# Kernel tuning notes

Measured on AMD Instinct MI355X. Metric: run time of the kernel, lower is better.

## Reference

```python
import jax, jax.numpy as jnp
import numpy as np

D_MODEL = 1024
D_HIDDEN = 4096
D_OUT = 1024
N_EXPERTS = 8
TOP_K = 2
LOAD_BALANCE_WEIGHT = 0.01


def setup_inputs() -> dict:
    key = jax.random.key(0)
    ks = jax.random.split(key, 8)
    s = 0.02
    return {
        "input_tensor": jax.random.normal(ks[0], (4, 2048, D_MODEL), dtype=jnp.float32),
        "router_w": jax.random.normal(ks[1], (N_EXPERTS, D_MODEL), dtype=jnp.float32) * s,
        "router_b": jnp.zeros((N_EXPERTS,), dtype=jnp.float32),
        "w1": jax.random.normal(ks[2], (N_EXPERTS, D_HIDDEN, D_MODEL), dtype=jnp.float32) * s,
        "b1": jnp.zeros((N_EXPERTS, D_HIDDEN), dtype=jnp.float32),
        "w2": jax.random.normal(ks[3], (N_EXPERTS, D_OUT, D_HIDDEN), dtype=jnp.float32) * s,
        "b2": jnp.zeros((N_EXPERTS, D_OUT), dtype=jnp.float32),
    }


def _moe(input_tensor, router_w, router_b, w1, b1, w2, b2):
    B, S, D = input_tensor.shape
    x = input_tensor.reshape(-1, D)  # [T, D]
    T = x.shape[0]

    router_logits = x @ router_w.T + router_b          # [T, E]
    router_probs = jax.nn.softmax(router_logits, -1)   # [T, E]
    topk_w, topk_idx = jax.lax.top_k(router_probs, TOP_K)  # [T, K]
    topk_w = topk_w / jnp.sum(topk_w, axis=-1, keepdims=True)

    # Dense combine weights: zero for unselected experts (same math as
    # gather/scatter loop since unselected contributions get weight 0).
    combine = jnp.zeros((T, N_EXPERTS), dtype=topk_w.dtype)
    combine = combine.at[jnp.arange(T)[:, None], topk_idx].add(topk_w)  # [T, E]

    out = jnp.zeros((T, D_OUT), dtype=x.dtype)
    for e in range(N_EXPERTS):  # fixed, small expert loop
        h = jax.nn.relu(x @ w1[e].T + b1[e])      # [T, H]
        y = h @ w2[e].T + b2[e]                   # [T, O]
        out = out + combine[:, e:e + 1] * y
    output = out.reshape(B, S, D_OUT)

    # Load-balance loss
    one_hot = jax.nn.one_hot(topk_idx, N_EXPERTS, dtype=router_probs.dtype)  # [T, K, E]
    usage_frac = jnp.sum(one_hot, axis=(0, 1)) / (T * TOP_K)                 # [E]
    mean_prob = jnp.mean(router_probs, axis=0)                               # [E]
    lb_loss = LOAD_BALANCE_WEIGHT * N_EXPERTS * jnp.sum(usage_frac * mean_prob)
    return output, lb_loss


def reference(input_tensor, router_w, router_b, w1, b1, w2, b2):
    return _moe(input_tensor, router_w, router_b, w1, b1, w2, b2)
```

## Files before the change

kernel.cpp:

```cpp
#include <hip/hip_runtime.h>

typedef unsigned short u16;
typedef __bf16 bf16x8 __attribute__((ext_vector_type(8)));
typedef float f32x4 __attribute__((ext_vector_type(4)));

#define T_TOKENS 8192
#define DM 1024
#define DH 4096
#define DO 1024
#define NE 8

#define XB_OFF   0ull
#define W1B_OFF  16777216ull
#define W2B_OFF  16777216ull
#define H_OFF    83886080ull
#define PT_OFF   218103808ull
#define PG_OFF   218169344ull
#define TI_OFF   218234880ull
#define TG_OFF   218300416ull
#define ST_OFF   218365952ull


typedef __attribute__((address_space(3))) void lds_void;
typedef __attribute__((address_space(1))) const void gbl_void;

__device__ __forceinline__ void gload_lds16(const void* g, void* l) {
  __builtin_amdgcn_global_load_lds((gbl_void*)g, (lds_void*)l, 16, 0, 0);
}

__device__ __forceinline__ u16 f2bf(float f) {
  union { float f; unsigned u; } a; a.f = f;
  unsigned u = a.u;
  return (u16)((u + 0x7FFFu + ((u >> 16) & 1u)) >> 16);
}

__global__ __launch_bounds__(256) void cast_f32_bf16(const float* __restrict__ src,
                                                     u16* __restrict__ dst, int n4) {
  int i = blockIdx.x * 256 + threadIdx.x;
  if (i >= n4) return;
  float4 v = ((const float4*)src)[i];
  ushort4 o;
  o.x = f2bf(v.x); o.y = f2bf(v.y); o.z = f2bf(v.z); o.w = f2bf(v.w);
  ((ushort4*)dst)[i] = o;
}

__global__ __launch_bounds__(256) void router_kernel(
    const float* __restrict__ x, const float* __restrict__ rw,
    const float* __restrict__ rb,
    int* __restrict__ tidx, float* __restrict__ tgate,
    int* __restrict__ counts, float* __restrict__ psum)
{
  __shared__ float srw[NE * DM];
  __shared__ float s_psum[NE];
  __shared__ int s_cnt[NE];

  for (int i = threadIdx.x; i < NE * DM; i += 256) srw[i] = rw[i];
  if (threadIdx.x < NE) { s_psum[threadIdx.x] = 0.f; s_cnt[threadIdx.x] = 0; }
  __syncthreads();

  const int wave = threadIdx.x >> 6;
  const int lane = threadIdx.x & 63;
  const int t = blockIdx.x * 4 + wave;

  float xv[16];
#pragma unroll
  for (int i = 0; i < 16; i++) xv[i] = x[(size_t)t * DM + i * 64 + lane];

  float logits[8];
#pragma unroll
  for (int e = 0; e < 8; e++) {
    float p = 0.f;
#pragma unroll
    for (int i = 0; i < 16; i++) p += xv[i] * srw[e * DM + i * 64 + lane];
#pragma unroll
    for (int o = 32; o > 0; o >>= 1) p += __shfl_xor(p, o, 64);
    logits[e] = p;
  }

  if (lane == 0) {
    float pe[8];
    float mx = -1e30f;
    for (int e = 0; e < 8; e++) { logits[e] += rb[e]; mx = fmaxf(mx, logits[e]); }
    float s = 0.f;
    for (int e = 0; e < 8; e++) { pe[e] = expf(logits[e] - mx); s += pe[e]; }
    float inv = 1.f / s;
    for (int e = 0; e < 8; e++) { pe[e] *= inv; atomicAdd(&s_psum[e], pe[e]); }
    int i0 = 0;
    for (int e = 1; e < 8; e++) if (pe[e] > pe[i0]) i0 = e;
    int i1 = (i0 == 0) ? 1 : 0;
    for (int e = 0; e < 8; e++) if (e != i0 && pe[e] > pe[i1]) i1 = e;
    float g = pe[i0] + pe[i1];
    tidx[t * 2] = i0; tidx[t * 2 + 1] = i1;
    tgate[t * 2] = pe[i0] / g; tgate[t * 2 + 1] = pe[i1] / g;
    atomicAdd(&s_cnt[i0], 1); atomicAdd(&s_cnt[i1], 1);
  }
  __syncthreads();
  if (threadIdx.x < NE) {
    atomicAdd(&counts[threadIdx.x], s_cnt[threadIdx.x]);
    atomicAdd(&psum[threadIdx.x], s_psum[threadIdx.x]);
  }
}

__global__ void offsets_kernel(const int* __restrict__ counts, int* __restrict__ offs) {
  if (threadIdx.x == 0) {
    int a = 0;
    for (int e = 0; e < NE; e++) { offs[e] = a; a += counts[e]; }
  }
}

__global__ __launch_bounds__(256) void scatter_kernel(
    const int* __restrict__ tidx, const float* __restrict__ tgate,
    const int* __restrict__ offs, int* __restrict__ cursor,
    int* __restrict__ ptok, float* __restrict__ pgate)
{
  int t = blockIdx.x * 256 + threadIdx.x;
#pragma unroll
  for (int k = 0; k < 2; k++) {
    int e = tidx[t * 2 + k];
    int pos = offs[e] + atomicAdd(&cursor[e], 1);
    ptok[pos] = t;
    pgate[pos] = tgate[t * 2 + k];
  }
}


#define GEMM_CORE_DECLS                                                        \
  __shared__ __align__(16) u16 sm[16384];        \
  const int tid = threadIdx.x;                                                 \
  const int lane = tid & 63;                                                   \
  const int wave = tid >> 6;                                                   \
  const int wm = wave & 1, wn = wave >> 1;                                     \
  const int q = lane >> 4, ml = lane & 15;                                     \
  const int schunk = (tid & 3) ^ ((tid >> 3) & 3);     \
  const int srow = tid >> 2;                                \
  const int fsw = (q ^ ((ml >> 1) & 3)) * 8;      \
  int offA[4], offB[4];                                                        \
  _Pragma("unroll") for (int t4 = 0; t4 < 4; t4++) {                           \
    offA[t4] = (wm * 64 + t4 * 16 + ml) * 32 + fsw;                            \
    offB[t4] = 4096 + (wn * 64 + t4 * 16 + ml) * 32 + fsw;                     \
  }                                                                            \
  const f32x4 z = {0.f, 0.f, 0.f, 0.f};                                        \
  f32x4 acc[4][4];                                                             \
  _Pragma("unroll") for (int i = 0; i < 4; i++)                                \
    _Pragma("unroll") for (int j = 0; j < 4; j++) acc[i][j] = z;

#define GEMM_STAGE(buf, k0)                                                    \
  {                                                                            \
    u16* dst = sm + (buf) * 8192 + tid * 8;                                    \
    gload_lds16(aptr0 + (k0), dst);                                            \
    gload_lds16(aptr1 + (k0), dst + 2048);                                     \
    gload_lds16(bptr0 + (k0), dst + 4096);                                     \
    gload_lds16(bptr1 + (k0), dst + 6144);                                     \
  }

#define GEMM_KLOOP(KD)                                                         \
  GEMM_STAGE(0, 0)                                                             \
  int cur = 0;                                                                 \
  for (int k0 = 0; k0 < (KD); k0 += 32) {                                      \
    __syncthreads();                                                           \
    if (k0 + 32 < (KD)) { GEMM_STAGE(cur ^ 1, k0 + 32) }                       \
    const u16* Ab = sm + cur * 8192;                                           \
    bf16x8 af[4], bv[4];                                                       \
    _Pragma("unroll") for (int mt = 0; mt < 4; mt++)                           \
      af[mt] = *(const bf16x8*)&Ab[offA[mt]];                                  \
    _Pragma("unroll") for (int nt = 0; nt < 4; nt++)                           \
      bv[nt] = *(const bf16x8*)&Ab[offB[nt]];                                  \
    _Pragma("unroll") for (int mt = 0; mt < 4; mt++)                           \
      _Pragma("unroll") for (int nt = 0; nt < 4; nt++)                         \
        acc[mt][nt] =                                                          \
            __builtin_amdgcn_mfma_f32_16x16x32_bf16(af[mt], bv[nt],            \
                                                    acc[mt][nt], 0, 0, 0);     \
    cur ^= 1;                                                                  \
  }

__global__ __launch_bounds__(256) void gemm1_kernel(
    const u16* __restrict__ xb, const u16* __restrict__ w1b,
    const float* __restrict__ b1, const int* __restrict__ ptok,
    const int* __restrict__ offs, const int* __restrict__ counts,
    u16* __restrict__ h)
{
  const int e = blockIdx.z;
  const int cnt = counts[e];
  const int row0 = blockIdx.y * 128;
  if (row0 >= cnt) return;
  const int off = offs[e];
  const int col0 = blockIdx.x * 128;

  GEMM_CORE_DECLS

  int ra0 = row0 + srow, ra1 = row0 + 64 + srow;
  int tk0 = ptok[off + (ra0 < cnt ? ra0 : 0)];
  int tk1 = ptok[off + (ra1 < cnt ? ra1 : 0)];
  const u16* aptr0 = xb + (size_t)tk0 * DM + schunk * 8;
  const u16* aptr1 = xb + (size_t)tk1 * DM + schunk * 8;
  const u16* bptr0 = w1b + ((size_t)e * DH + col0 + srow) * DM + schunk * 8;
  const u16* bptr1 = w1b + ((size_t)e * DH + col0 + 64 + srow) * DM + schunk * 8;

  GEMM_KLOOP(DM)

#pragma unroll
  for (int mt = 0; mt < 4; mt++) {
#pragma unroll
    for (int reg = 0; reg < 4; reg++) {
      int prow = row0 + wm * 64 + mt * 16 + q * 4 + reg;
      if (prow < cnt) {
#pragma unroll
        for (int nt = 0; nt < 4; nt++) {
          int gcol = col0 + wn * 64 + nt * 16 + ml;
          float v = acc[mt][nt][reg] + b1[e * DH + gcol];
          v = fmaxf(v, 0.f);
          h[(size_t)(off + prow) * DH + gcol] = f2bf(v);
        }
      }
    }
  }
}

__global__ __launch_bounds__(256) void gemm2_kernel(
    const u16* __restrict__ h, const u16* __restrict__ w2b,
    const float* __restrict__ b2, const int* __restrict__ ptok,
    const float* __restrict__ pgate,
    const int* __restrict__ offs, const int* __restrict__ counts,
    float* __restrict__ out)
{
  const int e = blockIdx.z;
  const int cnt = counts[e];
  const int row0 = blockIdx.y * 128;
  if (row0 >= cnt) return;
  const int off = offs[e];
  const int col0 = blockIdx.x * 128;

  GEMM_CORE_DECLS

  int ra0 = row0 + srow, ra1 = row0 + 64 + srow;
  int ar0 = off + (ra0 < cnt ? ra0 : 0);
  int ar1 = off + (ra1 < cnt ? ra1 : 0);
  const u16* aptr0 = h + (size_t)ar0 * DH + schunk * 8;
  const u16* aptr1 = h + (size_t)ar1 * DH + schunk * 8;
  const u16* bptr0 = w2b + ((size_t)e * DO + col0 + srow) * DH + schunk * 8;
  const u16* bptr1 = w2b + ((size_t)e * DO + col0 + 64 + srow) * DH + schunk * 8;

  GEMM_KLOOP(DH)

#pragma unroll
  for (int mt = 0; mt < 4; mt++) {
#pragma unroll
    for (int reg = 0; reg < 4; reg++) {
      int prow = row0 + wm * 64 + mt * 16 + q * 4 + reg;
      if (prow < cnt) {
        int t = ptok[off + prow];
        float g = pgate[off + prow];
#pragma unroll
        for (int nt = 0; nt < 4; nt++) {
          int gcol = col0 + wn * 64 + nt * 16 + ml;
          float v = acc[mt][nt][reg] + b2[e * DO + gcol];
          atomicAdd(&out[(size_t)t * DO + gcol], g * v);
        }
      }
    }
  }
}

__global__ void loss_kernel(const int* __restrict__ counts, const float* __restrict__ psum,
                            float* __restrict__ out, size_t idx, int T) {
  if (threadIdx.x == 0 && blockIdx.x == 0) {
    float s = 0.f;
    for (int e = 0; e < NE; e++)
      s += ((float)counts[e] / (float)(T * 2)) * (psum[e] / (float)T);
    out[idx] = 0.01f * 8.0f * s;
  }
}

extern "C" void kernel_launch(void* const* d_in, const int* in_sizes, int n_in,
                              void* d_out, int out_size, void* d_ws, size_t ws_size,
                              hipStream_t stream) {
  const float* x  = (const float*)d_in[0];
  const float* rw = (const float*)d_in[1];
  const float* rb = (const float*)d_in[2];
  const float* w1 = (const float*)d_in[3];
  const float* b1 = (const float*)d_in[4];
  const float* w2 = (const float*)d_in[5];
  const float* b2 = (const float*)d_in[6];
  float* out = (float*)d_out;
  char* ws = (char*)d_ws;

  u16* xb    = (u16*)(ws + XB_OFF);
  u16* w1b   = (u16*)(ws + W1B_OFF);
  u16* w2b   = (u16*)(ws + W2B_OFF);
  u16* h     = (u16*)(ws + H_OFF);
  int* ptok  = (int*)(ws + PT_OFF);
  float* pgate = (float*)(ws + PG_OFF);
  int* tidx  = (int*)(ws + TI_OFF);
  float* tgate = (float*)(ws + TG_OFF);
  int* counts = (int*)(ws + ST_OFF);
  int* cursor = (int*)(ws + ST_OFF + 32);
  int* offs   = (int*)(ws + ST_OFF + 64);
  float* psum = (float*)(ws + ST_OFF + 96);

  hipMemsetAsync(d_out, 0, (size_t)out_size * sizeof(float), stream);
  hipMemsetAsync(ws + ST_OFF, 0, 256, stream);

  cast_f32_bf16<<<(T_TOKENS * DM / 4 + 255) / 256, 256, 0, stream>>>(x, xb, T_TOKENS * DM / 4);
  cast_f32_bf16<<<(NE * DH * DM / 4 + 255) / 256, 256, 0, stream>>>(w1, w1b, NE * DH * DM / 4);

  router_kernel<<<T_TOKENS / 4, 256, 0, stream>>>(x, rw, rb, tidx, tgate, counts, psum);
  offsets_kernel<<<1, 64, 0, stream>>>(counts, offs);
  scatter_kernel<<<T_TOKENS / 256, 256, 0, stream>>>(tidx, tgate, offs, cursor, ptok, pgate);

  gemm1_kernel<<<dim3(DH / 128, T_TOKENS / 128, NE), 256, 0, stream>>>(
      xb, w1b, b1, ptok, offs, counts, h);

  cast_f32_bf16<<<(NE * DO * DH / 4 + 255) / 256, 256, 0, stream>>>(w2, w2b, NE * DO * DH / 4);

  gemm2_kernel<<<dim3(DO / 128, T_TOKENS / 128, NE), 256, 0, stream>>>(
      h, w2b, b2, ptok, pgate, offs, counts, out);

  loss_kernel<<<1, 1, 0, stream>>>(counts, psum, out, (size_t)out_size - 1, T_TOKENS);
}
```

Before: 911.4 us.

## Convert expert GEMMs to persistent grid-stride tile scheduling

Both expert GEMM kernels now launch a fixed grid of 1024 blocks. Each block loops over a flattened (expert, tile) index space and skips tiles beyond that expert's token count. The old 3D grid launched many blocks that exited immediately; this removes that launch and scheduling overhead. It also orders tiles column-major per expert and interleaves experts, which may change L2 reuse of weight tiles. The cost is that loop-carried LDS reuse between tiles depends on the buffer parity at the end of each K loop, and per-block load balance now depends on the routing counts.

```diff
diff --git a/kernel.cpp b/kernel.cpp
--- a/kernel.cpp
+++ b/kernel.cpp
@@ -9,6 +9,7 @@
 #define DH 4096
 #define DO 1024
 #define NE 8
+#define GRID_P 1024
 
 #define XB_OFF   0ull
 #define W1B_OFF  16777216ull
@@ -19,7 +20,6 @@
 #define TI_OFF   218234880ull
 #define TG_OFF   218300416ull
 #define ST_OFF   218365952ull
-
 
 typedef __attribute__((address_space(3))) void lds_void;
 typedef __attribute__((address_space(1))) const void gbl_void;
@@ -124,25 +124,21 @@
 }
 
 
-#define GEMM_CORE_DECLS                                                        \
+#define GEMM_PRE                                                               \
   __shared__ __align__(16) u16 sm[16384];        \
   const int tid = threadIdx.x;                                                 \
   const int lane = tid & 63;                                                   \
   const int wave = tid >> 6;                                                   \
   const int wm = wave & 1, wn = wave >> 1;                                     \
   const int q = lane >> 4, ml = lane & 15;                                     \
-  const int schunk = (tid & 3) ^ ((tid >> 3) & 3);     \
-  const int srow = tid >> 2;                                \
-  const int fsw = (q ^ ((ml >> 1) & 3)) * 8;      \
+  const int schunk = (tid & 3) ^ ((tid >> 3) & 3);                             \
+  const int srow = tid >> 2;                                        \
+  const int fsw = (q ^ ((ml >> 1) & 3)) * 8;                                   \
   int offA[4], offB[4];                                                        \
   _Pragma("unroll") for (int t4 = 0; t4 < 4; t4++) {                           \
     offA[t4] = (wm * 64 + t4 * 16 + ml) * 32 + fsw;                            \
     offB[t4] = 4096 + (wn * 64 + t4 * 16 + ml) * 32 + fsw;                     \
-  }                                                                            \
-  const f32x4 z = {0.f, 0.f, 0.f, 0.f};                                        \
-  f32x4 acc[4][4];                                                             \
-  _Pragma("unroll") for (int i = 0; i < 4; i++)                                \
-    _Pragma("unroll") for (int j = 0; j < 4; j++) acc[i][j] = z;
+  }
 
 #define GEMM_STAGE(buf, k0)                                                    \
   {                                                                            \
@@ -154,6 +150,10 @@
   }
 
 #define GEMM_KLOOP(KD)                                                         \
+  const f32x4 z = {0.f, 0.f, 0.f, 0.f};                                        \
+  f32x4 acc[4][4];                                                             \
+  _Pragma("unroll") for (int ii = 0; ii < 4; ii++)                             \
+    _Pragma("unroll") for (int jj = 0; jj < 4; jj++) acc[ii][jj] = z;          \
   GEMM_STAGE(0, 0)                                                             \
   int cur = 0;                                                                 \
   for (int k0 = 0; k0 < (KD); k0 += 32) {                                      \
@@ -179,37 +179,42 @@
     const int* __restrict__ offs, const int* __restrict__ counts,
     u16* __restrict__ h)
 {
-  const int e = blockIdx.z;
-  const int cnt = counts[e];
-  const int row0 = blockIdx.y * 128;
-  if (row0 >= cnt) return;
-  const int off = offs[e];
-  const int col0 = blockIdx.x * 128;
-
-  GEMM_CORE_DECLS
-
-  int ra0 = row0 + srow, ra1 = row0 + 64 + srow;
-  int tk0 = ptok[off + (ra0 < cnt ? ra0 : 0)];
-  int tk1 = ptok[off + (ra1 < cnt ? ra1 : 0)];
-  const u16* aptr0 = xb + (size_t)tk0 * DM + schunk * 8;
-  const u16* aptr1 = xb + (size_t)tk1 * DM + schunk * 8;
-  const u16* bptr0 = w1b + ((size_t)e * DH + col0 + srow) * DM + schunk * 8;
-  const u16* bptr1 = w1b + ((size_t)e * DH + col0 + 64 + srow) * DM + schunk * 8;
-
-  GEMM_KLOOP(DM)
-
-#pragma unroll
-  for (int mt = 0; mt < 4; mt++) {
-#pragma unroll
-    for (int reg = 0; reg < 4; reg++) {
-      int prow = row0 + wm * 64 + mt * 16 + q * 4 + reg;
-      if (prow < cnt) {
-#pragma unroll
-        for (int nt = 0; nt < 4; nt++) {
-          int gcol = col0 + wn * 64 + nt * 16 + ml;
-          float v = acc[mt][nt][reg] + b1[e * DH + gcol];
-          v = fmaxf(v, 0.f);
-          h[(size_t)(off + prow) * DH + gcol] = f2bf(v);
+  GEMM_PRE
+
+  for (int i = blockIdx.x; i < NE * 64 * 32; i += gridDim.x) {
+    const int e = i & 7;
+    const int j = i >> 3;
+    const int cnt = counts[e];
+    const int nrb = (cnt + 127) >> 7;
+    if (j >= nrb * 32) continue;
+    const int colb = j / nrb;
+    const int rowb = j - colb * nrb;
+    const int row0 = rowb * 128, col0 = colb * 128;
+    const int off = offs[e];
+
+    int ra0 = row0 + srow, ra1 = row0 + 64 + srow;
+    int tk0 = ptok[off + (ra0 < cnt ? ra0 : 0)];
+    int tk1 = ptok[off + (ra1 < cnt ? ra1 : 0)];
+    const u16* aptr0 = xb + (size_t)tk0 * DM + schunk * 8;
+    const u16* aptr1 = xb + (size_t)tk1 * DM + schunk * 8;
+    const u16* bptr0 = w1b + ((size_t)e * DH + col0 + srow) * DM + schunk * 8;
+    const u16* bptr1 = w1b + ((size_t)e * DH + col0 + 64 + srow) * DM + schunk * 8;
+
+    GEMM_KLOOP(DM)
+
+#pragma unroll
+    for (int mt = 0; mt < 4; mt++) {
+#pragma unroll
+      for (int reg = 0; reg < 4; reg++) {
+        int prow = row0 + wm * 64 + mt * 16 + q * 4 + reg;
+        if (prow < cnt) {
+#pragma unroll
+          for (int nt = 0; nt < 4; nt++) {
+            int gcol = col0 + wn * 64 + nt * 16 + ml;
+            float v = acc[mt][nt][reg] + b1[e * DH + gcol];
+            v = fmaxf(v, 0.f);
+            h[(size_t)(off + prow) * DH + gcol] = f2bf(v);
+          }
         }
       }
     }
@@ -223,38 +228,43 @@
     const int* __restrict__ offs, const int* __restrict__ counts,
     float* __restrict__ out)
 {
-  const int e = blockIdx.z;
-  const int cnt = counts[e];
-  const int row0 = blockIdx.y * 128;
-  if (row0 >= cnt) return;
-  const int off = offs[e];
-  const int col0 = blockIdx.x * 128;
-
-  GEMM_CORE_DECLS
-
-  int ra0 = row0 + srow, ra1 = row0 + 64 + srow;
-  int ar0 = off + (ra0 < cnt ? ra0 : 0);
-  int ar1 = off + (ra1 < cnt ? ra1 : 0);
-  const u16* aptr0 = h + (size_t)ar0 * DH + schunk * 8;
-  const u16* aptr1 = h + (size_t)ar1 * DH + schunk * 8;
-  const u16* bptr0 = w2b + ((size_t)e * DO + col0 + srow) * DH + schunk * 8;
-  const u16* bptr1 = w2b + ((size_t)e * DO + col0 + 64 + srow) * DH + schunk * 8;
-
-  GEMM_KLOOP(DH)
-
-#pragma unroll
-  for (int mt = 0; mt < 4; mt++) {
-#pragma unroll
-    for (int reg = 0; reg < 4; reg++) {
-      int prow = row0 + wm * 64 + mt * 16 + q * 4 + reg;
-      if (prow < cnt) {
-        int t = ptok[off + prow];
-        float g = pgate[off + prow];
-#pragma unroll
-        for (int nt = 0; nt < 4; nt++) {
-          int gcol = col0 + wn * 64 + nt * 16 + ml;
-          float v = acc[mt][nt][reg] + b2[e * DO + gcol];
-          atomicAdd(&out[(size_t)t * DO + gcol], g * v);
+  GEMM_PRE
+
+  for (int i = blockIdx.x; i < NE * 64 * 8; i += gridDim.x) {
+    const int e = i & 7;
+    const int j = i >> 3;
+    const int cnt = counts[e];
+    const int nrb = (cnt + 127) >> 7;
+    if (j >= nrb * 8) continue;
+    const int colb = j / nrb;
+    const int rowb = j - colb * nrb;
+    const int row0 = rowb * 128, col0 = colb * 128;
+    const int off = offs[e];
+
+    int ra0 = row0 + srow, ra1 = row0 + 64 + srow;
+    int ar0 = off + (ra0 < cnt ? ra0 : 0);
+    int ar1 = off + (ra1 < cnt ? ra1 : 0);
+    const u16* aptr0 = h + (size_t)ar0 * DH + schunk * 8;
+    const u16* aptr1 = h + (size_t)ar1 * DH + schunk * 8;
+    const u16* bptr0 = w2b + ((size_t)e * DO + col0 + srow) * DH + schunk * 8;
+    const u16* bptr1 = w2b + ((size_t)e * DO + col0 + 64 + srow) * DH + schunk * 8;
+
+    GEMM_KLOOP(DH)
+
+#pragma unroll
+    for (int mt = 0; mt < 4; mt++) {
+#pragma unroll
+      for (int reg = 0; reg < 4; reg++) {
+        int prow = row0 + wm * 64 + mt * 16 + q * 4 + reg;
+        if (prow < cnt) {
+          int t = ptok[off + prow];
+          float g = pgate[off + prow];
+#pragma unroll
+          for (int nt = 0; nt < 4; nt++) {
+            int gcol = col0 + wn * 64 + nt * 16 + ml;
+            float v = acc[mt][nt][reg] + b2[e * DO + gcol];
+            atomicAdd(&out[(size_t)t * DO + gcol], g * v);
+          }
         }
       }
     }
@@ -307,13 +317,11 @@
   offsets_kernel<<<1, 64, 0, stream>>>(counts, offs);
   scatter_kernel<<<T_TOKENS / 256, 256, 0, stream>>>(tidx, tgate, offs, cursor, ptok, pgate);
 
-  gemm1_kernel<<<dim3(DH / 128, T_TOKENS / 128, NE), 256, 0, stream>>>(
-      xb, w1b, b1, ptok, offs, counts, h);
+  gemm1_kernel<<<GRID_P, 256, 0, stream>>>(xb, w1b, b1, ptok, offs, counts, h);
 
   cast_f32_bf16<<<(NE * DO * DH / 4 + 255) / 256, 256, 0, stream>>>(w2, w2b, NE * DO * DH / 4);
 
-  gemm2_kernel<<<dim3(DO / 128, T_TOKENS / 128, NE), 256, 0, stream>>>(
-      h, w2b, b2, ptok, pgate, offs, counts, out);
+  gemm2_kernel<<<GRID_P, 256, 0, stream>>>(h, w2b, b2, ptok, pgate, offs, counts, out);
 
   loss_kernel<<<1, 1, 0, stream>>>(counts, psum, out, (size_t)out_size - 1, T_TOKENS);
 }
```

After: 974.0 us. 6.9% more time.
